# Kernel tuning notes

Hardware: AMD Instinct MI355X
Metric: run time of the kernel (lower is better)

Reference implementation:

```python
import jax, jax.numpy as jnp
import numpy as np


def setup_inputs() -> dict:
    key = jax.random.key(0)
    k1, k2 = jax.random.split(key)
    B, P, C, N = 32, 3, 512, 1024
    input_data1 = jax.random.normal(k1, (B, P, C, N), dtype=jnp.float32)
    input_data2 = jax.random.normal(k2, (B, P, C, N), dtype=jnp.float32)
    return {"input_data1": input_data1, "input_data2": input_data2}


def reference(input_data1, input_data2):
    # HorizontalComparisonModel.compare_algorithm_method4 (the only path used):
    # permute [B,P,C,N] -> [B,P,N,C], reshape to [B, P*N, C] pairs of C-dim vectors.
    B = input_data1.shape[0]
    x = jnp.transpose(input_data1, (0, 1, 3, 2)).reshape(B, -1, input_data1.shape[2])
    y = jnp.transpose(input_data2, (0, 1, 3, 2)).reshape(B, -1, input_data2.shape[2])
    d = x - y                                   # [B, pairs, C]
    l1 = jnp.sum(jnp.abs(d), axis=-1)           # temp31: L1 distance
    sq_l2 = jnp.sum(d * d, axis=-1)             # temp21: squared L2 distance
    # Original stacks [temp31, temp21, temp31] (L1 appears twice; cosine unused).
    out = jnp.stack([l1, sq_l2, l1], axis=-1)   # [B, pairs, 3]
    return out.reshape(B, -1)
```

## Files before the change

kernel.cpp:

```cpp
#include <hip/hip_runtime.h>

constexpr int B = 32, P = 3, C = 512, N = 1024;
constexpr int G = B * P;

template <int CS>
__global__ __launch_bounds__(256) void dist_partial(
    const float* __restrict__ x1, const float* __restrict__ x2,
    float* __restrict__ ws)
{
    constexpr int ROWS = C / CS;
    const int g     = blockIdx.x / CS;
    const int chunk = blockIdx.x % CS;
    const int t     = threadIdx.x;

    const float4* pa = (const float4*)(x1 + (size_t)g * C * N)
                       + (size_t)chunk * (N / 4) + t;
    const float4* pb = (const float4*)(x2 + (size_t)g * C * N)
                       + (size_t)chunk * (N / 4) + t;
    constexpr size_t RSTRIDE = (size_t)CS * (N / 4);

    float4 l1 = make_float4(0.f, 0.f, 0.f, 0.f);
    float4 l2 = make_float4(0.f, 0.f, 0.f, 0.f);

    #pragma unroll
    for (int j = 0; j < ROWS; j += 4) {
        const float4 a0 = pa[(j + 0) * RSTRIDE];
        const float4 a1 = pa[(j + 1) * RSTRIDE];
        const float4 a2 = pa[(j + 2) * RSTRIDE];
        const float4 a3 = pa[(j + 3) * RSTRIDE];
        const float4 b0 = pb[(j + 0) * RSTRIDE];
        const float4 b1 = pb[(j + 1) * RSTRIDE];
        const float4 b2 = pb[(j + 2) * RSTRIDE];
        const float4 b3 = pb[(j + 3) * RSTRIDE];
        float d;
        d = a0.x - b0.x; l1.x += fabsf(d); l2.x = fmaf(d, d, l2.x);
        d = a0.y - b0.y; l1.y += fabsf(d); l2.y = fmaf(d, d, l2.y);
        d = a0.z - b0.z; l1.z += fabsf(d); l2.z = fmaf(d, d, l2.z);
        d = a0.w - b0.w; l1.w += fabsf(d); l2.w = fmaf(d, d, l2.w);
        d = a1.x - b1.x; l1.x += fabsf(d); l2.x = fmaf(d, d, l2.x);
        d = a1.y - b1.y; l1.y += fabsf(d); l2.y = fmaf(d, d, l2.y);
        d = a1.z - b1.z; l1.z += fabsf(d); l2.z = fmaf(d, d, l2.z);
        d = a1.w - b1.w; l1.w += fabsf(d); l2.w = fmaf(d, d, l2.w);
        d = a2.x - b2.x; l1.x += fabsf(d); l2.x = fmaf(d, d, l2.x);
        d = a2.y - b2.y; l1.y += fabsf(d); l2.y = fmaf(d, d, l2.y);
        d = a2.z - b2.z; l1.z += fabsf(d); l2.z = fmaf(d, d, l2.z);
        d = a2.w - b2.w; l1.w += fabsf(d); l2.w = fmaf(d, d, l2.w);
        d = a3.x - b3.x; l1.x += fabsf(d); l2.x = fmaf(d, d, l2.x);
        d = a3.y - b3.y; l1.y += fabsf(d); l2.y = fmaf(d, d, l2.y);
        d = a3.z - b3.z; l1.z += fabsf(d); l2.z = fmaf(d, d, l2.z);
        d = a3.w - b3.w; l1.w += fabsf(d); l2.w = fmaf(d, d, l2.w);
    }

    float4* wout = (float4*)ws + ((size_t)(chunk * G + g) * N) / 2 + 2 * t;
    wout[0] = make_float4(l1.x, l2.x, l1.y, l2.y);
    wout[1] = make_float4(l1.z, l2.z, l1.w, l2.w);
}

template <int CS>
__global__ __launch_bounds__(256) void dist_combine(
    const float* __restrict__ ws, float* __restrict__ out)
{
    const int idx = blockIdx.x * 256 + threadIdx.x;
    const float2* ws2 = (const float2*)ws;
    float l1 = 0.f, l2 = 0.f;
    #pragma unroll
    for (int chunk = 0; chunk < CS; ++chunk) {
        const float2 v = ws2[(size_t)chunk * G * N + idx];
        l1 += v.x;
        l2 += v.y;
    }
    out[3 * (size_t)idx + 0] = l1;
    out[3 * (size_t)idx + 1] = l2;
    out[3 * (size_t)idx + 2] = l1;
}

__global__ __launch_bounds__(256) void dist_atomic(
    const float* __restrict__ x1, const float* __restrict__ x2,
    float* __restrict__ out)
{
    constexpr int CS = 16;
    const int g     = blockIdx.x / CS;
    const int chunk = blockIdx.x % CS;
    const int t     = threadIdx.x;
    const float4* a = (const float4*)(x1 + (size_t)g * C * N) + t;
    const float4* b = (const float4*)(x2 + (size_t)g * C * N) + t;
    float4 l1 = make_float4(0.f, 0.f, 0.f, 0.f);
    float4 l2 = make_float4(0.f, 0.f, 0.f, 0.f);
    for (int j = 0; j < C / CS; ++j) {
        const int c = chunk + CS * j;
        const float4 av = a[(size_t)c * (N / 4)];
        const float4 bv = b[(size_t)c * (N / 4)];
        float d;
        d = av.x - bv.x; l1.x += fabsf(d); l2.x = fmaf(d, d, l2.x);
        d = av.y - bv.y; l1.y += fabsf(d); l2.y = fmaf(d, d, l2.y);
        d = av.z - bv.z; l1.z += fabsf(d); l2.z = fmaf(d, d, l2.z);
        d = av.w - bv.w; l1.w += fabsf(d); l2.w = fmaf(d, d, l2.w);
    }
    const size_t obase = ((size_t)g * N + 4 * (size_t)t) * 3;
    const float l1v[4] = {l1.x, l1.y, l1.z, l1.w};
    const float l2v[4] = {l2.x, l2.y, l2.z, l2.w};
    #pragma unroll
    for (int i = 0; i < 4; ++i) {
        atomicAdd(&out[obase + 3 * i + 0], l1v[i]);
        atomicAdd(&out[obase + 3 * i + 1], l2v[i]);
        atomicAdd(&out[obase + 3 * i + 2], l1v[i]);
    }
}

extern "C" void kernel_launch(void* const* d_in, const int* in_sizes, int n_in,
                              void* d_out, int out_size, void* d_ws, size_t ws_size,
                              hipStream_t stream) {
    const float* x1 = (const float*)d_in[0];
    const float* x2 = (const float*)d_in[1];
    float* out = (float*)d_out;

    const size_t need32 = (size_t)32 * G * N * 2 * sizeof(float);
    const size_t need16 = (size_t)16 * G * N * 2 * sizeof(float);

    if (ws_size >= need32) {
        dist_partial<32><<<G * 32, 256, 0, stream>>>(x1, x2, (float*)d_ws);
        dist_combine<32><<<(G * N) / 256, 256, 0, stream>>>((const float*)d_ws, out);
    } else if (ws_size >= need16) {
        dist_partial<16><<<G * 16, 256, 0, stream>>>(x1, x2, (float*)d_ws);
        dist_combine<16><<<(G * N) / 256, 256, 0, stream>>>((const float*)d_ws, out);
    } else {
        hipMemsetAsync(d_out, 0, (size_t)out_size * sizeof(float), stream);
        dist_atomic<<<G * 16, 256, 0, stream>>>(x1, x2, out);
    }
}
```

Baseline: 393.9 us.

## Fuse partial and combine kernels via last-block counter reduction

Replaces the two-kernel partial-sum plus combine scheme with a single kernel. The last block to finish for each group, detected with an atomic counter, sums the per-chunk partials and writes the interleaved output as float4 stores. It also fixes the chunk split at 16 and makes each chunk read a contiguous band of rows instead of a strided set, improving locality. The cost is a memset of the counters, threadfences, and a serial combine tail done by a few blocks.

```diff
diff --git a/kernel.cpp b/kernel.cpp
--- a/kernel.cpp
+++ b/kernel.cpp
@@ -2,36 +2,37 @@
 
 constexpr int B = 32, P = 3, C = 512, N = 1024;
 constexpr int G = B * P;
+constexpr int CS = 16;
+constexpr int ROWS = C / CS;
+constexpr size_t CNT_PAD = 4096;
+constexpr size_t WS_NEED = CNT_PAD + (size_t)CS * G * N * 2 * sizeof(float);
 
-template <int CS>
-__global__ __launch_bounds__(256) void dist_partial(
+__global__ __launch_bounds__(256) void dist_fused(
     const float* __restrict__ x1, const float* __restrict__ x2,
-    float* __restrict__ ws)
+    float* __restrict__ ws_part, int* __restrict__ cnt,
+    float* __restrict__ out)
 {
-    constexpr int ROWS = C / CS;
     const int g     = blockIdx.x / CS;
     const int chunk = blockIdx.x % CS;
     const int t     = threadIdx.x;
 
-    const float4* pa = (const float4*)(x1 + (size_t)g * C * N)
-                       + (size_t)chunk * (N / 4) + t;
-    const float4* pb = (const float4*)(x2 + (size_t)g * C * N)
-                       + (size_t)chunk * (N / 4) + t;
-    constexpr size_t RSTRIDE = (size_t)CS * (N / 4);
+    const size_t base = (size_t)g * C * N + (size_t)chunk * ROWS * N;
+    const float4* pa = (const float4*)(x1 + base) + t;
+    const float4* pb = (const float4*)(x2 + base) + t;
 
     float4 l1 = make_float4(0.f, 0.f, 0.f, 0.f);
     float4 l2 = make_float4(0.f, 0.f, 0.f, 0.f);
 
     #pragma unroll
     for (int j = 0; j < ROWS; j += 4) {
-        const float4 a0 = pa[(j + 0) * RSTRIDE];
-        const float4 a1 = pa[(j + 1) * RSTRIDE];
-        const float4 a2 = pa[(j + 2) * RSTRIDE];
-        const float4 a3 = pa[(j + 3) * RSTRIDE];
-        const float4 b0 = pb[(j + 0) * RSTRIDE];
-        const float4 b1 = pb[(j + 1) * RSTRIDE];
-        const float4 b2 = pb[(j + 2) * RSTRIDE];
-        const float4 b3 = pb[(j + 3) * RSTRIDE];
+        const float4 a0 = pa[(j + 0) * (N / 4)];
+        const float4 a1 = pa[(j + 1) * (N / 4)];
+        const float4 a2 = pa[(j + 2) * (N / 4)];
+        const float4 a3 = pa[(j + 3) * (N / 4)];
+        const float4 b0 = pb[(j + 0) * (N / 4)];
+        const float4 b1 = pb[(j + 1) * (N / 4)];
+        const float4 b2 = pb[(j + 2) * (N / 4)];
+        const float4 b3 = pb[(j + 3) * (N / 4)];
         float d;
         d = a0.x - b0.x; l1.x += fabsf(d); l2.x = fmaf(d, d, l2.x);
         d = a0.y - b0.y; l1.y += fabsf(d); l2.y = fmaf(d, d, l2.y);
@@ -51,34 +52,41 @@
         d = a3.w - b3.w; l1.w += fabsf(d); l2.w = fmaf(d, d, l2.w);
     }
 
-    float4* wout = (float4*)ws + ((size_t)(chunk * G + g) * N) / 2 + 2 * t;
+    float4* wout = (float4*)ws_part + ((size_t)(chunk * G + g) * N) / 2 + 2 * t;
     wout[0] = make_float4(l1.x, l2.x, l1.y, l2.y);
     wout[1] = make_float4(l1.z, l2.z, l1.w, l2.w);
-}
 
-template <int CS>
-__global__ __launch_bounds__(256) void dist_combine(
-    const float* __restrict__ ws, float* __restrict__ out)
-{
-    const int idx = blockIdx.x * 256 + threadIdx.x;
-    const float2* ws2 = (const float2*)ws;
-    float l1 = 0.f, l2 = 0.f;
+    __shared__ int winner;
+    __threadfence();
+    if (t == 0) {
+        const int old = atomicAdd(&cnt[g], 1);
+        winner = (old == CS - 1);
+    }
+    __syncthreads();
+    if (!winner) return;
+    __threadfence();
+
+    float4 acc0 = make_float4(0.f, 0.f, 0.f, 0.f);
+    float4 acc1 = make_float4(0.f, 0.f, 0.f, 0.f);
     #pragma unroll
-    for (int chunk = 0; chunk < CS; ++chunk) {
-        const float2 v = ws2[(size_t)chunk * G * N + idx];
-        l1 += v.x;
-        l2 += v.y;
+    for (int c = 0; c < CS; ++c) {
+        const float4* p = (const float4*)ws_part
+                          + ((size_t)(c * G + g) * N) / 2 + 2 * t;
+        const float4 v0 = p[0];
+        const float4 v1 = p[1];
+        acc0.x += v0.x; acc0.y += v0.y; acc0.z += v0.z; acc0.w += v0.w;
+        acc1.x += v1.x; acc1.y += v1.y; acc1.z += v1.z; acc1.w += v1.w;
     }
-    out[3 * (size_t)idx + 0] = l1;
-    out[3 * (size_t)idx + 1] = l2;
-    out[3 * (size_t)idx + 2] = l1;
+    float4* obase = (float4*)out + (size_t)768 * g + 3 * t;
+    obase[0] = make_float4(acc0.x, acc0.y, acc0.x, acc0.z);
+    obase[1] = make_float4(acc0.w, acc0.z, acc1.x, acc1.y);
+    obase[2] = make_float4(acc1.x, acc1.z, acc1.w, acc1.z);
 }
 
 __global__ __launch_bounds__(256) void dist_atomic(
     const float* __restrict__ x1, const float* __restrict__ x2,
     float* __restrict__ out)
 {
-    constexpr int CS = 16;
     const int g     = blockIdx.x / CS;
     const int chunk = blockIdx.x % CS;
     const int t     = threadIdx.x;
@@ -86,8 +94,8 @@
     const float4* b = (const float4*)(x2 + (size_t)g * C * N) + t;
     float4 l1 = make_float4(0.f, 0.f, 0.f, 0.f);
     float4 l2 = make_float4(0.f, 0.f, 0.f, 0.f);
-    for (int j = 0; j < C / CS; ++j) {
-        const int c = chunk + CS * j;
+    for (int j = 0; j < ROWS; ++j) {
+        const int c = chunk * ROWS + j;
         const float4 av = a[(size_t)c * (N / 4)];
         const float4 bv = b[(size_t)c * (N / 4)];
         float d;
@@ -114,17 +122,13 @@
     const float* x2 = (const float*)d_in[1];
     float* out = (float*)d_out;
 
-    const size_t need32 = (size_t)32 * G * N * 2 * sizeof(float);
-    const size_t need16 = (size_t)16 * G * N * 2 * sizeof(float);
-
-    if (ws_size >= need32) {
-        dist_partial<32><<<G * 32, 256, 0, stream>>>(x1, x2, (float*)d_ws);
-        dist_combine<32><<<(G * N) / 256, 256, 0, stream>>>((const float*)d_ws, out);
-    } else if (ws_size >= need16) {
-        dist_partial<16><<<G * 16, 256, 0, stream>>>(x1, x2, (float*)d_ws);
-        dist_combine<16><<<(G * N) / 256, 256, 0, stream>>>((const float*)d_ws, out);
+    if (ws_size >= WS_NEED) {
+        int*   cnt  = (int*)d_ws;
+        float* part = (float*)((char*)d_ws + CNT_PAD);
+        hipMemsetAsync(cnt, 0, G * sizeof(int), stream);
+        dist_fused<<<G * CS, 256, 0, stream>>>(x1, x2, part, cnt, out);
     } else {
         hipMemsetAsync(d_out, 0, (size_t)out_size * sizeof(float), stream);
-        dist_atomic<<<G * 16, 256, 0, stream>>>(x1, x2, out);
+        dist_atomic<<<G * CS, 256, 0, stream>>>(x1, x2, out);
     }
 }
```

After: 777.7 us. 97.4% more time.
